# Kernel optimization log

Hardware: AMD Instinct MI355X
Metric: run time of the kernel (lower is better)

The kernel has to match this reference:

```python
import jax, jax.numpy as jnp
import numpy as np

# Dims: M=batch, T=time frames, B=bottleneck channels, H=intermediate channels, KK=kernel size
M, T, B, H, KK = 8, 4000, 128, 512, 3
DILATION = 2
EPS = 1e-8  # gLN eps (ConvTasNet convention)


def prelu(x, a):
    return jnp.where(x >= 0, x, a * x)


def gln(x, gamma, beta):
    # global layer norm over (time, channel) per sample; x: [M, T, C]
    m = jnp.mean(x, axis=(1, 2), keepdims=True)
    v = jnp.mean((x - m) ** 2, axis=(1, 2), keepdims=True)
    return gamma * (x - m) / jnp.sqrt(v + EPS) + beta


def depthwise_conv_same_reflect(x, w):
    # x: [M, C, L], w: [C, K]; dilation 1, 'same' padding with reflect mode
    K = w.shape[1]
    pl = (K - 1) // 2
    xp = jnp.pad(x, ((0, 0), (0, 0), (pl, K - 1 - pl)), mode='reflect')
    return jax.lax.conv_general_dilated(
        xp, w[:, None, :], (1,), 'VALID',
        feature_group_count=x.shape[1], dimension_numbers=('NCH', 'OIH', 'NCH'))


def setup_inputs() -> dict:
    key = jax.random.key(0)
    ks = jax.random.split(key, 12)
    f32 = jnp.float32
    return {
        'x': jax.random.normal(ks[0], (M, T, B), f32),
        'conv1_w': jax.random.normal(ks[1], (H, B), f32) * 0.05,
        'prelu1_a': jnp.asarray(0.25, f32),
        'norm1_g': jnp.ones((H,), f32),
        'norm1_b': jnp.zeros((H,), f32),
        'off_dw_w': jax.random.normal(ks[2], (H, KK), f32) * 0.02,
        'odc_prelu_a': jnp.asarray(0.25, f32),
        'off_pw_w': jax.random.normal(ks[3], (KK, H), f32) * 0.02,
        'opc_prelu_a': jnp.asarray(0.25, f32),
        'dw_w': jax.random.normal(ks[4], (H, KK), f32) * 0.05,
        'dw_b': jax.random.normal(ks[5], (H,), f32) * 0.01,
        'prelu2_a': jnp.asarray(0.25, f32),
        'norm2_g': jnp.ones((H,), f32),
        'norm2_b': jnp.zeros((H,), f32),
        'pw_w': jax.random.normal(ks[6], (B, H), f32) * 0.05,
    }


def reference(x, conv1_w, prelu1_a, norm1_g, norm1_b,
              off_dw_w, odc_prelu_a, off_pw_w, opc_prelu_a,
              dw_w, dw_b, prelu2_a, norm2_g, norm2_b, pw_w):
    dtype = x.dtype
    residual = x
    # 1x1 bottleneck conv -> PReLU -> gLN
    h = jnp.einsum('mtb,hb->mth', x, conv1_w)
    h = gln(prelu(h, prelu1_a), norm1_g, norm1_b)
    hc = jnp.moveaxis(h, 1, 2)  # [M, H, T]

    # --- offset prediction branch (PackedDeformConv1d) ---
    off = depthwise_conv_same_reflect(hc, off_dw_w)          # [M, H, T]
    off = prelu(off, odc_prelu_a)
    off = jnp.einsum('mct,kc->mkt', off, off_pw_w)           # [M, KK, T]
    off = prelu(off, opc_prelu_a)
    offsets = jnp.moveaxis(off, 1, 2)                        # [M, T, KK]

    # --- deformable depthwise conv (same padding, reflect) ---
    pad_tot = DILATION * (KK - 1)
    pl = pad_tot // 2
    xp = jnp.pad(hc, ((0, 0), (0, 0), (pl, pad_tot - pl)), mode='reflect')  # [M,H,Lp]
    Lp = T + pad_tot
    dil_pos = (jnp.arange(KK) * DILATION).astype(dtype)      # [KK]: 0, d, 2d
    t0 = jnp.arange(T, dtype=dtype)[:, None]                 # [T,1]
    Tpos = t0 + dil_pos[None, :] + offsets                   # [M,T,KK]
    Tpos = jnp.clip(Tpos, t0, t0 + dil_pos[-1])              # constrain to receptive field
    U = jnp.clip(jnp.floor(Tpos).astype(jnp.int32), 0, Lp - 2)
    Uf = U.astype(dtype)
    g0 = jax.nn.relu(1.0 - jnp.abs(Uf - Tpos))               # [M,T,KK]
    g1 = jax.nn.relu(1.0 - jnp.abs(Uf + 1.0 - Tpos))
    idx = jnp.broadcast_to(U.reshape(M, 1, T * KK), (M, H, T * KK))
    s0 = jnp.take_along_axis(xp, idx, axis=2).reshape(M, H, T, KK)
    s1 = jnp.take_along_axis(xp, idx + 1, axis=2).reshape(M, H, T, KK)
    sampled = g0[:, None] * s0 + g1[:, None] * s1            # [M,H,T,KK]
    y = jnp.einsum('mhtk,hk->mht', sampled, dw_w) + dw_b[None, :, None]

    # PReLU -> gLN -> 1x1 conv back to B channels, residual add
    y = jnp.moveaxis(y, 1, 2)                                # [M,T,H]
    y = gln(prelu(y, prelu2_a), norm2_g, norm2_b)
    out = jnp.einsum('mth,bh->mtb', y, pw_w)
    return out + residual
```

## Files before the change

### kernel.cpp

```cpp
#include <hip/hip_runtime.h>

#define Mdim 8
#define Tdim 4000
#define Bdim 128
#define Hdim 512
#define NPER (Tdim*Hdim)
#define EPSG 1e-8f
#define ROWS 69

typedef __attribute__((ext_vector_type(8))) short short8;
typedef __attribute__((ext_vector_type(4))) float floatx4;

static __device__ __forceinline__ float bits2f(unsigned short s) {
  union { unsigned int u; float f; } v; v.u = ((unsigned int)s) << 16; return v.f;
}
static __device__ __forceinline__ unsigned short f2bits(float f) {
  union { float f; unsigned int u; } v; v.f = f;
  unsigned int u = v.u;
  u += 0x7fffu + ((u >> 16) & 1u);
  return (unsigned short)(u >> 16);
}
static __device__ __forceinline__ short8 pack8(const float4& a, const float4& b) {
  short8 v;
  v[0]=(short)f2bits(a.x); v[1]=(short)f2bits(a.y); v[2]=(short)f2bits(a.z); v[3]=(short)f2bits(a.w);
  v[4]=(short)f2bits(b.x); v[5]=(short)f2bits(b.y); v[6]=(short)f2bits(b.z); v[7]=(short)f2bits(b.w);
  return v;
}

#define LDS_FENCE() do { \
  asm volatile("s_waitcnt lgkmcnt(0)" ::: "memory"); \
  __builtin_amdgcn_sched_barrier(0); \
} while (0)

__global__ __launch_bounds__(256) void k_prep(
    const float* __restrict__ w1, unsigned short* __restrict__ w1r)
{
  int i = blockIdx.x*256 + threadIdx.x;
  int lane = i & 63, f = i >> 6;
  int nt = f & 3, ks = (f >> 2) & 3, hc = f >> 4;
  int h = hc*64 + nt*16 + (lane & 15);
  int c = ks*32 + (lane >> 4)*8;
  const float* src = &w1[(size_t)h*Bdim + c];
  float4 a = *(const float4*)src;
  float4 b = *(const float4*)(src + 4);
  *(short8*)&w1r[(size_t)i*8] = pack8(a, b);
}

__global__ __launch_bounds__(256) void k_conv1(
    const float* __restrict__ x,
    const unsigned short* __restrict__ w1r,
    const float* __restrict__ a1p,
    unsigned short* __restrict__ Hbuf,
    float2* __restrict__ part1)
{
  __shared__ __align__(16) unsigned short ltile[64*72];
  __shared__ float red[512];

  const int tid = threadIdx.x;
  const int t0 = blockIdx.x * 64;
  const int m  = blockIdx.y;
  const int lane = tid & 63, wv = tid >> 6, quad = lane >> 4, l16 = lane & 15;
  int tr = t0 + wv*16 + l16;
  int trc = tr < Tdim ? tr : Tdim-1;
  const float* xrow = x + ((size_t)m*Tdim + trc)*Bdim;
  short8 afr[4];
  #pragma unroll
  for (int ks = 0; ks < 4; ++ks) {
    float4 fa = *(const float4*)&xrow[ks*32 + quad*8];
    float4 fb = *(const float4*)&xrow[ks*32 + quad*8 + 4];
    afr[ks] = pack8(fa, fb);
  }

  const float a1 = a1p[0];
  const short8* wf = (const short8*)w1r + lane;
  float lsum = 0.f, lss = 0.f;

  for (int hc = 0; hc < 8; ++hc) {
    floatx4 acc[4] = {};
    #pragma unroll
    for (int ks = 0; ks < 4; ++ks)
      #pragma unroll
      for (int nt = 0; nt < 4; ++nt)
        acc[nt] = __builtin_amdgcn_mfma_f32_16x16x32_bf16(
            afr[ks], wf[(hc*16 + ks*4 + nt)*64], acc[nt], 0, 0, 0);

    #pragma unroll
    for (int nt = 0; nt < 4; ++nt) {
      int hl = nt*16 + l16;
      #pragma unroll
      for (int r = 0; r < 4; ++r) {
        int tl = wv*16 + quad*4 + r;
        float v = acc[nt][r];
        v = v >= 0.f ? v : a1 * v;
        if (t0 + tl < Tdim) { lsum += v; lss += v*v; }
        ltile[tl*72 + hl] = f2bits(v);
      }
    }
    LDS_FENCE();
    {
      int tr2 = tid >> 2, ck = (tid & 3) * 16;
      int tg = t0 + tr2;
      if (tg < Tdim) {
        unsigned short* dst = &Hbuf[((size_t)m*Tdim + tg)*Hdim + hc*64 + ck];
        *(short8*)&dst[0] = *(const short8*)&ltile[tr2*72 + ck];
        *(short8*)&dst[8] = *(const short8*)&ltile[tr2*72 + ck + 8];
      }
    }
    LDS_FENCE();
  }

  red[tid] = lsum; red[256 + tid] = lss;
  __syncthreads();
  for (int s = 128; s > 0; s >>= 1) {
    if (tid < s) { red[tid] += red[tid + s]; red[256+tid] += red[256+tid+s]; }
    __syncthreads();
  }
  if (tid == 0)
    part1[(size_t)m*63 + blockIdx.x] = make_float2(red[0], red[256]);
}

__global__ __launch_bounds__(256) void k_deform(
    const unsigned short* __restrict__ Hbuf,
    const float2* __restrict__ part1,
    const float* __restrict__ g1w,
    const float* __restrict__ b1w,
    const float* __restrict__ odw,
    const float* __restrict__ aodcp,
    const float* __restrict__ opw,
    const float* __restrict__ aopcp,
    const float* __restrict__ dww,
    const float* __restrict__ dwb,
    const float* __restrict__ a2p,
    unsigned short* __restrict__ Ybuf,
    float2* __restrict__ part2)
{
  __shared__ __align__(16) unsigned short tile[ROWS*512];
  __shared__ float s_stats[2];
  __shared__ float rsum[4], rss[4];
  const int tid = threadIdx.x, lane = tid & 63, w = tid >> 6;
  const int t0 = blockIdx.x * 64;
  const int m = blockIdx.y;
  const int c8 = lane*8;
  const unsigned short* base = Hbuf + (size_t)m*Tdim*Hdim;

  short8 stg[17];
  #pragma unroll
  for (int i = 0; i < 17; ++i) {
    int s = t0 - 2 + w + i*4;
    s = s < 0 ? -s : s;
    if (s > Tdim-1) s = 2*(Tdim-1) - s;
    stg[i] = *(const short8*)&base[(size_t)s*Hdim + c8];
  }
  short8 extra;
  if (w == 0) {
    int s = t0 + 66;
    if (s > Tdim-1) s = 2*(Tdim-1) - s;
    extra = *(const short8*)&base[(size_t)s*Hdim + c8];
  }

  if (tid < 64) {
    float s = 0.f, q = 0.f;
    if (lane < 63) { float2 p = part1[(size_t)m*63 + lane]; s = p.x; q = p.y; }
    #pragma unroll
    for (int st = 32; st > 0; st >>= 1) { s += __shfl_xor(s, st); q += __shfl_xor(q, st); }
    if (lane == 0) { s_stats[0] = s; s_stats[1] = q; }
  }

  #pragma unroll
  for (int i = 0; i < 17; ++i)
    *(short8*)&tile[(w + i*4)*512 + c8] = stg[i];
  if (w == 0) *(short8*)&tile[68*512 + c8] = extra;

  __syncthreads();

  const float invn = 1.0f/(float)NPER;
  const float mean1 = s_stats[0]*invn;
  const float var1  = fmaxf(s_stats[1]*invn - mean1*mean1, 0.f);
  const float inv1  = 1.0f/sqrtf(var1 + EPSG);

  const float aodc = aodcp[0], aopc = aopcp[0], a2 = a2p[0];
  float wod[24], q0v[8], q1v[8], q2v[8], wd[24], bv[8], Ax[8], Cx[8];
  #pragma unroll
  for (int j = 0; j < 8; j += 4) {
    *(float4*)&q0v[j] = *(const float4*)&opw[c8 + j];
    *(float4*)&q1v[j] = *(const float4*)&opw[Hdim + c8 + j];
    *(float4*)&q2v[j] = *(const float4*)&opw[2*Hdim + c8 + j];
    *(float4*)&bv[j]  = *(const float4*)&dwb[c8 + j];
  }
  #pragma unroll
  for (int j = 0; j < 24; j += 4) {
    *(float4*)&wod[j] = *(const float4*)&odw[c8*3 + j];
    *(float4*)&wd[j]  = *(const float4*)&dww[c8*3 + j];
  }
  #pragma unroll
  for (int j = 0; j < 8; ++j) {
    Ax[j] = g1w[c8 + j] * inv1;
    Cx[j] = b1w[c8 + j] - mean1*Ax[j];
  }

  float lsum = 0.f, lss = 0.f;
  #pragma unroll 1
  for (int it = 0; it < 16; it += 2) {
    const int t = t0 + w*16 + it;
    if (t >= Tdim) break;
    const int sb = t - t0 + 2;

    short8 hrow[2][3];
    #pragma unroll
    for (int tt = 0; tt < 2; ++tt)
      #pragma unroll
      for (int k = 0; k < 3; ++k)
        hrow[tt][k] = *(const short8*)&tile[(sb + tt - 1 + k)*512 + c8];

    float oa[2][3] = {};
    #pragma unroll
    for (int j = 0; j < 8; ++j) {
      float A = Ax[j], C = Cx[j];
      #pragma unroll
      for (int tt = 0; tt < 2; ++tt) {
        float fm = fmaf(A, bits2f((unsigned short)hrow[tt][0][j]), C);
        float fz = fmaf(A, bits2f((unsigned short)hrow[tt][1][j]), C);
        float fp = fmaf(A, bits2f((unsigned short)hrow[tt][2][j]), C);
        float d = fm*wod[j*3+0] + fz*wod[j*3+1] + fp*wod[j*3+2];
        d = d >= 0.f ? d : aodc*d;
        oa[tt][0] = fmaf(d, q0v[j], oa[tt][0]);
        oa[tt][1] = fmaf(d, q1v[j], oa[tt][1]);
        oa[tt][2] = fmaf(d, q2v[j], oa[tt][2]);
      }
    }
    #pragma unroll
    for (int st = 32; st > 0; st >>= 1) {
      #pragma unroll
      for (int tt = 0; tt < 2; ++tt) {
        oa[tt][0] += __shfl_xor(oa[tt][0], st);
        oa[tt][1] += __shfl_xor(oa[tt][1], st);
        oa[tt][2] += __shfl_xor(oa[tt][2], st);
      }
    }

    int S0[2][3], S1[2][3]; float G0[2][3], G1[2][3], GS[2][3];
    #pragma unroll
    for (int tt = 0; tt < 2; ++tt) {
      const float tf = (float)(t + tt);
      #pragma unroll
      for (int k = 0; k < 3; ++k) {
        float off = oa[tt][k];
        off = off >= 0.f ? off : aopc*off;
        float pos = tf + (float)(2*k) + off;
        pos = fminf(fmaxf(pos, tf), tf + 4.0f);
        int U = (int)floorf(pos);
        if (U > Tdim + 2) U = Tdim + 2;
        float Uf = (float)U;
        G0[tt][k] = fmaxf(0.f, 1.f - fabsf(Uf - pos));
        G1[tt][k] = fmaxf(0.f, 1.f - fabsf(Uf + 1.f - pos));
        GS[tt][k] = G0[tt][k] + G1[tt][k];
        S0[tt][k] = U - t0;
        S1[tt][k] = U - t0 + 1;
      }
    }

    short8 s0v[2][3], s1v[2][3];
    #pragma unroll
    for (int tt = 0; tt < 2; ++tt)
      #pragma unroll
      for (int k = 0; k < 3; ++k) {
        s0v[tt][k] = *(const short8*)&tile[S0[tt][k]*512 + c8];
        s1v[tt][k] = *(const short8*)&tile[S1[tt][k]*512 + c8];
      }

    short8 yv[2];
    #pragma unroll
    for (int j = 0; j < 8; ++j) {
      float A = Ax[j], C = Cx[j];
      float w0 = wd[j*3+0], w1 = wd[j*3+1], w2 = wd[j*3+2];
      #pragma unroll
      for (int tt = 0; tt < 2; ++tt) {
        float ybase = fmaf(C, w0*GS[tt][0] + w1*GS[tt][1] + w2*GS[tt][2], bv[j]);
        float t0s = fmaf(G1[tt][0], bits2f((unsigned short)s1v[tt][0][j]), G0[tt][0]*bits2f((unsigned short)s0v[tt][0][j]));
        float t1s = fmaf(G1[tt][1], bits2f((unsigned short)s1v[tt][1][j]), G0[tt][1]*bits2f((unsigned short)s0v[tt][1][j]));
        float t2s = fmaf(G1[tt][2], bits2f((unsigned short)s1v[tt][2][j]), G0[tt][2]*bits2f((unsigned short)s0v[tt][2][j]));
        float acc2 = w0*t0s + w1*t1s + w2*t2s;
        float y = fmaf(A, acc2, ybase);
        float p = y >= 0.f ? y : a2*y;
        lsum += p; lss += p*p;
        yv[tt][j] = (short)f2bits(p);
      }
    }
    #pragma unroll
    for (int tt = 0; tt < 2; ++tt)
      *(short8*)&Ybuf[((size_t)m*Tdim + t + tt)*Hdim + c8] = yv[tt];
  }

  #pragma unroll
  for (int st = 32; st > 0; st >>= 1) {
    lsum += __shfl_xor(lsum, st);
    lss  += __shfl_xor(lss, st);
  }
  if (lane == 0) { rsum[w] = lsum; rss[w] = lss; }
  __syncthreads();
  if (tid == 0)
    part2[(size_t)m*63 + blockIdx.x] =
      make_float2(rsum[0]+rsum[1]+rsum[2]+rsum[3], rss[0]+rss[1]+rss[2]+rss[3]);
}

__global__ __launch_bounds__(64) void k_w2(
    const float2* __restrict__ part2,
    const float* __restrict__ g2w,
    const float* __restrict__ b2w,
    const float* __restrict__ pww,
    unsigned short* __restrict__ W2r,
    float* __restrict__ const2)
{
  const int bid = blockIdx.x;
  const int m = bid >> 7, b = bid & 127;
  const int tid = threadIdx.x;

  float s = 0.f, q = 0.f;
  if (tid < 63) { float2 p = part2[(size_t)m*63 + tid]; s = p.x; q = p.y; }
  #pragma unroll
  for (int st = 32; st > 0; st >>= 1) { s += __shfl_xor(s, st); q += __shfl_xor(q, st); }

  const float invn = 1.0f/(float)NPER;
  const float mean2 = s*invn;
  const float var2  = fmaxf(q*invn - mean2*mean2, 0.f);
  const float inv2  = 1.0f/sqrtf(var2 + EPSG);

  const int j8 = tid*8;
  float g2v[8], b2v[8], pv[8];
  #pragma unroll
  for (int j = 0; j < 8; j += 4) {
    *(float4*)&g2v[j] = *(const float4*)&g2w[j8 + j];
    *(float4*)&b2v[j] = *(const float4*)&b2w[j8 + j];
    *(float4*)&pv[j]  = *(const float4*)&pww[(size_t)b*Hdim + j8 + j];
  }
  float csum = 0.f;
  short8 wv8;
  #pragma unroll
  for (int j = 0; j < 8; ++j) {
    float A = g2v[j] * inv2;
    float C = b2v[j] - mean2*A;
    csum = fmaf(C, pv[j], csum);
    wv8[j] = (short)f2bits(A*pv[j]);
  }
  {
    int half = b >> 6, nt = (b >> 4) & 3, l16 = b & 15;
    int kc = tid >> 4, ks = (tid >> 2) & 3, quad = tid & 3;
    int lane = quad*16 + l16;
    size_t f = ((((size_t)(m*2 + half)*4 + kc)*4 + ks)*4 + nt);
    *(short8*)&W2r[(f*64 + lane)*8] = wv8;
  }

  #pragma unroll
  for (int st = 32; st > 0; st >>= 1) csum += __shfl_down(csum, st);
  if (tid == 0) const2[m*Bdim + b] = csum;
}

__global__ __launch_bounds__(256) void k_out(
    const unsigned short* __restrict__ Ybuf,
    const unsigned short* __restrict__ W2r,
    const float* __restrict__ const2,
    const float* __restrict__ x,
    float* __restrict__ out)
{
  __shared__ __align__(16) float ltf[64*68];
  const int tid = threadIdx.x;
  const int t0 = blockIdx.x*64;
  const int half = blockIdx.y;
  const int n0 = half*64;
  const int m  = blockIdx.z;
  const int lane = tid & 63, wv = tid >> 6, quad = lane >> 4, l16 = lane & 15;
  int tr = t0 + wv*16 + l16;
  int trc = tr < Tdim ? tr : Tdim-1;
  const unsigned short* arow = Ybuf + ((size_t)m*Tdim + trc)*Hdim;
  const short8* wf = (const short8*)W2r + (size_t)(m*2 + half)*64*64 + lane;

  floatx4 acc[4] = {};
  #pragma unroll
  for (int kc = 0; kc < 4; ++kc)
    #pragma unroll
    for (int ks = 0; ks < 4; ++ks) {
      short8 afr = *(const short8*)&arow[kc*128 + ks*32 + quad*8];
      #pragma unroll
      for (int nt = 0; nt < 4; ++nt)
        acc[nt] = __builtin_amdgcn_mfma_f32_16x16x32_bf16(
            afr, wf[((kc*4 + ks)*4 + nt)*64], acc[nt], 0, 0, 0);
    }

  #pragma unroll
  for (int nt = 0; nt < 4; ++nt) {
    int bl = nt*16 + l16;
    float cb = const2[m*Bdim + n0 + bl];
    #pragma unroll
    for (int r = 0; r < 4; ++r) {
      int tl = wv*16 + quad*4 + r;
      ltf[tl*68 + bl] = acc[nt][r] + cb;
    }
  }
  LDS_FENCE();
  {
    int tr2 = tid >> 2, ck = (tid & 3) * 16;
    int tg = t0 + tr2;
    if (tg < Tdim) {
      const float* xr = &x[((size_t)m*Tdim + tg)*Bdim + n0 + ck];
      float* orow = &out[((size_t)m*Tdim + tg)*Bdim + n0 + ck];
      #pragma unroll
      for (int j = 0; j < 4; ++j) {
        float4 v = *(const float4*)&ltf[tr2*68 + ck + j*4];
        float4 rx = *(const float4*)&xr[j*4];
        v.x += rx.x; v.y += rx.y; v.z += rx.z; v.w += rx.w;
        *(float4*)&orow[j*4] = v;
      }
    }
  }
}

extern "C" void kernel_launch(void* const* d_in, const int* in_sizes, int n_in,
                              void* d_out, int out_size, void* d_ws, size_t ws_size,
                              hipStream_t stream)
{
  (void)in_sizes; (void)n_in; (void)out_size; (void)ws_size;
  const float* x    = (const float*)d_in[0];
  const float* w1   = (const float*)d_in[1];
  const float* a1   = (const float*)d_in[2];
  const float* g1   = (const float*)d_in[3];
  const float* b1   = (const float*)d_in[4];
  const float* odw  = (const float*)d_in[5];
  const float* aodc = (const float*)d_in[6];
  const float* opw  = (const float*)d_in[7];
  const float* aopc = (const float*)d_in[8];
  const float* dww  = (const float*)d_in[9];
  const float* dwb  = (const float*)d_in[10];
  const float* a2   = (const float*)d_in[11];
  const float* g2   = (const float*)d_in[12];
  const float* b2   = (const float*)d_in[13];
  const float* pww  = (const float*)d_in[14];
  float* out = (float*)d_out;

  char* ws = (char*)d_ws;
  const size_t OFF_P1  = 0;
  const size_t OFF_C2  = 4096;
  const size_t OFF_P2  = 8192;
  const size_t OFF_W1R = 12288;
  const size_t OFF_W2  = 143360;
  const size_t OFF_H   = 1191936;
  const size_t OFF_Y   = 33959936;
  float2* part1  = (float2*)(ws + OFF_P1);
  float*  const2 = (float*)(ws + OFF_C2);
  float2* part2  = (float2*)(ws + OFF_P2);
  unsigned short* w1r  = (unsigned short*)(ws + OFF_W1R);
  unsigned short* W2r  = (unsigned short*)(ws + OFF_W2);
  unsigned short* Hbuf = (unsigned short*)(ws + OFF_H);
  unsigned short* Ybuf = (unsigned short*)(ws + OFF_Y);

  k_prep  <<<dim3(32), 256, 0, stream>>>(w1, w1r);
  k_conv1 <<<dim3(63, 8), 256, 0, stream>>>(x, w1r, a1, Hbuf, part1);
  k_deform<<<dim3(63, 8), 256, 0, stream>>>(Hbuf, part1, g1, b1, odw, aodc, opw, aopc, dww, dwb, a2, Ybuf, part2);
  k_w2    <<<dim3(1024), 64, 0, stream>>>(part2, g2, b2, pww, W2r, const2);
  k_out   <<<dim3(63, 2, 8), 256, 0, stream>>>(Ybuf, W2r, const2, x, out);
}
```

Baseline: 169.9 us.

## Split deformable stage into offset-MFMA and sampling kernels with more blocks

The monolithic deform kernel is split into a per-sample stats kernel, an offset-prediction kernel that runs the 512-to-3 pointwise projection on MFMA with precomputed folded weights, and a sampling kernel gridded at 500 blocks per sample that reads taps from a buffer and gathers directly from global memory. conv1 is also regridded to 32-row tiles (125 blocks per sample) with per-wave LDS tiles, raising parallelism and dropping the shuffle-heavy reductions. The cost is extra launches, a taps buffer round-trip, and unshared global gathers instead of an LDS tile.

```diff
diff --git a/kernel.cpp b/kernel.cpp
--- a/kernel.cpp
+++ b/kernel.cpp
@@ -6,7 +6,6 @@
 #define Hdim 512
 #define NPER (Tdim*Hdim)
 #define EPSG 1e-8f
-#define ROWS 69
 
 typedef __attribute__((ext_vector_type(8))) short short8;
 typedef __attribute__((ext_vector_type(4))) float floatx4;
@@ -33,17 +32,35 @@
 } while (0)
 
 __global__ __launch_bounds__(256) void k_prep(
-    const float* __restrict__ w1, unsigned short* __restrict__ w1r)
-{
-  int i = blockIdx.x*256 + threadIdx.x;
-  int lane = i & 63, f = i >> 6;
-  int nt = f & 3, ks = (f >> 2) & 3, hc = f >> 4;
-  int h = hc*64 + nt*16 + (lane & 15);
-  int c = ks*32 + (lane >> 4)*8;
-  const float* src = &w1[(size_t)h*Bdim + c];
-  float4 a = *(const float4*)src;
-  float4 b = *(const float4*)(src + 4);
-  *(short8*)&w1r[(size_t)i*8] = pack8(a, b);
+    const float* __restrict__ w1, const float* __restrict__ opw,
+    unsigned short* __restrict__ w1r, unsigned short* __restrict__ opwr)
+{
+  const int tid = threadIdx.x;
+  if (blockIdx.x < 32) {
+    int i = blockIdx.x*256 + tid;
+    int lane = i & 63, f = i >> 6;
+    int nt = f & 3, ks = (f >> 2) & 3, hc = f >> 4;
+    int h = hc*64 + nt*16 + (lane & 15);
+    int c = ks*32 + (lane >> 4)*8;
+    const float* src = &w1[(size_t)h*Bdim + c];
+    float4 a = *(const float4*)src;
+    float4 b = *(const float4*)(src + 4);
+    *(short8*)&w1r[(size_t)i*8] = pack8(a, b);
+  } else {
+    #pragma unroll
+    for (int it = 0; it < 4; ++it) {
+      int idx = it*256 + tid;
+      int ks = idx >> 6, lane = idx & 63;
+      int l16 = lane & 15, q = lane >> 4;
+      int h = ks*32 + q*8;
+      float4 a = make_float4(0.f,0.f,0.f,0.f), b = a;
+      if (l16 < 3) {
+        a = *(const float4*)&opw[(size_t)l16*Hdim + h];
+        b = *(const float4*)&opw[(size_t)l16*Hdim + h + 4];
+      }
+      *(short8*)&opwr[(size_t)idx*8] = pack8(a, b);
+    }
+  }
 }
 
 __global__ __launch_bounds__(256) void k_conv1(
@@ -53,16 +70,16 @@
     unsigned short* __restrict__ Hbuf,
     float2* __restrict__ part1)
 {
-  __shared__ __align__(16) unsigned short ltile[64*72];
+  __shared__ __align__(16) unsigned short ltile[4][16*72];
   __shared__ float red[512];
 
   const int tid = threadIdx.x;
-  const int t0 = blockIdx.x * 64;
+  const int t0 = blockIdx.x * 32;
   const int m  = blockIdx.y;
-  const int lane = tid & 63, wv = tid >> 6, quad = lane >> 4, l16 = lane & 15;
-  int tr = t0 + wv*16 + l16;
-  int trc = tr < Tdim ? tr : Tdim-1;
-  const float* xrow = x + ((size_t)m*Tdim + trc)*Bdim;
+  const int lane = tid & 63, w = tid >> 6, quad = lane >> 4, l16 = lane & 15;
+  const int tsub = w & 1, hh = w >> 1;
+  const int tbase = t0 + tsub*16;
+  const float* xrow = x + ((size_t)m*Tdim + tbase + l16)*Bdim;
   short8 afr[4];
   #pragma unroll
   for (int ks = 0; ks < 4; ++ks) {
@@ -75,36 +92,35 @@
   const short8* wf = (const short8*)w1r + lane;
   float lsum = 0.f, lss = 0.f;
 
-  for (int hc = 0; hc < 8; ++hc) {
+  #pragma unroll
+  for (int hc4 = 0; hc4 < 4; ++hc4) {
+    const int hcg = hh*4 + hc4;
     floatx4 acc[4] = {};
     #pragma unroll
     for (int ks = 0; ks < 4; ++ks)
       #pragma unroll
       for (int nt = 0; nt < 4; ++nt)
         acc[nt] = __builtin_amdgcn_mfma_f32_16x16x32_bf16(
-            afr[ks], wf[(hc*16 + ks*4 + nt)*64], acc[nt], 0, 0, 0);
+            afr[ks], wf[(hcg*16 + ks*4 + nt)*64], acc[nt], 0, 0, 0);
 
     #pragma unroll
     for (int nt = 0; nt < 4; ++nt) {
       int hl = nt*16 + l16;
       #pragma unroll
       for (int r = 0; r < 4; ++r) {
-        int tl = wv*16 + quad*4 + r;
+        int tl = quad*4 + r;
         float v = acc[nt][r];
         v = v >= 0.f ? v : a1 * v;
-        if (t0 + tl < Tdim) { lsum += v; lss += v*v; }
-        ltile[tl*72 + hl] = f2bits(v);
+        lsum += v; lss += v*v;
+        ltile[w][tl*72 + hl] = f2bits(v);
       }
     }
     LDS_FENCE();
     {
-      int tr2 = tid >> 2, ck = (tid & 3) * 16;
-      int tg = t0 + tr2;
-      if (tg < Tdim) {
-        unsigned short* dst = &Hbuf[((size_t)m*Tdim + tg)*Hdim + hc*64 + ck];
-        *(short8*)&dst[0] = *(const short8*)&ltile[tr2*72 + ck];
-        *(short8*)&dst[8] = *(const short8*)&ltile[tr2*72 + ck + 8];
-      }
+      int row = lane >> 2, ck = (lane & 3) * 16;
+      unsigned short* dst = &Hbuf[((size_t)m*Tdim + tbase + row)*Hdim + hcg*64 + ck];
+      *(short8*)&dst[0] = *(const short8*)&ltile[w][row*72 + ck];
+      *(short8*)&dst[8] = *(const short8*)&ltile[w][row*72 + ck + 8];
     }
     LDS_FENCE();
   }
@@ -116,180 +132,188 @@
     __syncthreads();
   }
   if (tid == 0)
-    part1[(size_t)m*63 + blockIdx.x] = make_float2(red[0], red[256]);
-}
-
-__global__ __launch_bounds__(256) void k_deform(
-    const unsigned short* __restrict__ Hbuf,
+    part1[(size_t)m*125 + blockIdx.x] = make_float2(red[0], red[256]);
+}
+
+__global__ __launch_bounds__(128) void k_stats1(
     const float2* __restrict__ part1,
     const float* __restrict__ g1w,
     const float* __restrict__ b1w,
     const float* __restrict__ odw,
+    float2* __restrict__ axcx,
+    float4* __restrict__ wodc)
+{
+  const int m = blockIdx.x, tid = threadIdx.x, lane = tid & 63, w = tid >> 6;
+  __shared__ float sh[4];
+  float s = 0.f, q = 0.f;
+  if (tid < 125) { float2 p = part1[(size_t)m*125 + tid]; s = p.x; q = p.y; }
+  #pragma unroll
+  for (int st = 32; st > 0; st >>= 1) { s += __shfl_xor(s, st); q += __shfl_xor(q, st); }
+  if (lane == 0) { sh[w*2] = s; sh[w*2+1] = q; }
+  __syncthreads();
+  const float S = sh[0] + sh[2], Q = sh[1] + sh[3];
+  const float invn = 1.0f/(float)NPER;
+  const float mean1 = S*invn;
+  const float var1  = fmaxf(Q*invn - mean1*mean1, 0.f);
+  const float inv1  = 1.0f/sqrtf(var1 + EPSG);
+  #pragma unroll
+  for (int i = 0; i < 4; ++i) {
+    int h = tid*4 + i;
+    float A = g1w[h]*inv1;
+    float C = b1w[h] - mean1*A;
+    axcx[(size_t)m*Hdim + h] = make_float2(A, C);
+    float w0 = odw[h*3], w1_ = odw[h*3+1], w2 = odw[h*3+2];
+    wodc[(size_t)m*Hdim + h] = make_float4(A*w0, A*w1_, A*w2, C*(w0+w1_+w2));
+  }
+}
+
+__global__ __launch_bounds__(256) void k_offs(
+    const unsigned short* __restrict__ Hbuf,
+    const float4* __restrict__ wodc,
+    const unsigned short* __restrict__ opwr,
     const float* __restrict__ aodcp,
-    const float* __restrict__ opw,
     const float* __restrict__ aopcp,
+    float4* __restrict__ taps)
+{
+  const int tid = threadIdx.x, lane = tid & 63, w = tid >> 6;
+  const int quad = lane >> 4, l16 = lane & 15;
+  const int m = blockIdx.y;
+  const int tbase = blockIdx.x*64 + w*16;
+  int t = tbase + l16;
+  int tc = t < Tdim ? t : Tdim-1;
+  int tm1 = tc == 0 ? 1 : tc-1;
+  int tp1 = tc == Tdim-1 ? Tdim-2 : tc+1;
+  const unsigned short* r0p = Hbuf + ((size_t)m*Tdim + tm1)*Hdim;
+  const unsigned short* r1p = Hbuf + ((size_t)m*Tdim + tc )*Hdim;
+  const unsigned short* r2p = Hbuf + ((size_t)m*Tdim + tp1)*Hdim;
+  const float4* wcb = wodc + (size_t)m*Hdim;
+  const float aodc = aodcp[0], aopc = aopcp[0];
+
+  floatx4 acc = {};
+  #pragma unroll
+  for (int g = 0; g < 4; ++g) {
+    short8 h0v[4], h1v[4], h2v[4], bop[4];
+    #pragma unroll
+    for (int k2 = 0; k2 < 4; ++k2) {
+      int hc = (g*4 + k2)*32 + quad*8;
+      h0v[k2] = *(const short8*)&r0p[hc];
+      h1v[k2] = *(const short8*)&r1p[hc];
+      h2v[k2] = *(const short8*)&r2p[hc];
+      bop[k2] = *(const short8*)&opwr[(size_t)((g*4 + k2)*64 + lane)*8];
+    }
+    #pragma unroll
+    for (int k2 = 0; k2 < 4; ++k2) {
+      int hc = (g*4 + k2)*32 + quad*8;
+      float d[8];
+      #pragma unroll
+      for (int j = 0; j < 8; ++j) {
+        float4 wc = wcb[hc + j];
+        float dv = fmaf(wc.x, bits2f((unsigned short)h0v[k2][j]),
+                   fmaf(wc.y, bits2f((unsigned short)h1v[k2][j]),
+                   fmaf(wc.z, bits2f((unsigned short)h2v[k2][j]), wc.w)));
+        d[j] = dv >= 0.f ? dv : aodc*dv;
+      }
+      short8 afr = pack8(make_float4(d[0],d[1],d[2],d[3]),
+                         make_float4(d[4],d[5],d[6],d[7]));
+      acc = __builtin_amdgcn_mfma_f32_16x16x32_bf16(afr, bop[k2], acc, 0, 0, 0);
+    }
+  }
+
+  if (l16 < 3) {
+    #pragma unroll
+    for (int r = 0; r < 4; ++r) {
+      int tout = tbase + quad*4 + r;
+      if (tout < Tdim) {
+        float off = acc[r];
+        off = off >= 0.f ? off : aopc*off;
+        float tf = (float)tout;
+        float pos = tf + (float)(2*l16) + off;
+        pos = fminf(fmaxf(pos, tf), tf + 4.0f);
+        int U = (int)floorf(pos);
+        if (U > Tdim + 2) U = Tdim + 2;
+        float Uf = (float)U;
+        float g0 = fmaxf(0.f, 1.f - fabsf(Uf - pos));
+        float g1 = fmaxf(0.f, 1.f - fabsf(Uf + 1.f - pos));
+        int ia = U - 2; ia = ia < 0 ? -ia : ia; if (ia > Tdim-1) ia = 2*(Tdim-1) - ia;
+        int ib = U - 1; ib = ib < 0 ? -ib : ib; if (ib > Tdim-1) ib = 2*(Tdim-1) - ib;
+        taps[((size_t)m*Tdim + tout)*3 + l16] =
+            make_float4(g0, g1, __int_as_float(ia), __int_as_float(ib));
+      }
+    }
+  }
+}
+
+__global__ __launch_bounds__(256) void k_samp(
+    const unsigned short* __restrict__ Hbuf,
+    const float4* __restrict__ taps,
+    const float2* __restrict__ axcx,
     const float* __restrict__ dww,
     const float* __restrict__ dwb,
     const float* __restrict__ a2p,
     unsigned short* __restrict__ Ybuf,
     float2* __restrict__ part2)
 {
-  __shared__ __align__(16) unsigned short tile[ROWS*512];
-  __shared__ float s_stats[2];
   __shared__ float rsum[4], rss[4];
   const int tid = threadIdx.x, lane = tid & 63, w = tid >> 6;
-  const int t0 = blockIdx.x * 64;
+  const int tb = blockIdx.x*8 + w*2;
   const int m = blockIdx.y;
   const int c8 = lane*8;
   const unsigned short* base = Hbuf + (size_t)m*Tdim*Hdim;
 
-  short8 stg[17];
-  #pragma unroll
-  for (int i = 0; i < 17; ++i) {
-    int s = t0 - 2 + w + i*4;
-    s = s < 0 ? -s : s;
-    if (s > Tdim-1) s = 2*(Tdim-1) - s;
-    stg[i] = *(const short8*)&base[(size_t)s*Hdim + c8];
-  }
-  short8 extra;
-  if (w == 0) {
-    int s = t0 + 66;
-    if (s > Tdim-1) s = 2*(Tdim-1) - s;
-    extra = *(const short8*)&base[(size_t)s*Hdim + c8];
-  }
-
-  if (tid < 64) {
-    float s = 0.f, q = 0.f;
-    if (lane < 63) { float2 p = part1[(size_t)m*63 + lane]; s = p.x; q = p.y; }
-    #pragma unroll
-    for (int st = 32; st > 0; st >>= 1) { s += __shfl_xor(s, st); q += __shfl_xor(q, st); }
-    if (lane == 0) { s_stats[0] = s; s_stats[1] = q; }
-  }
-
-  #pragma unroll
-  for (int i = 0; i < 17; ++i)
-    *(short8*)&tile[(w + i*4)*512 + c8] = stg[i];
-  if (w == 0) *(short8*)&tile[68*512 + c8] = extra;
-
-  __syncthreads();
-
-  const float invn = 1.0f/(float)NPER;
-  const float mean1 = s_stats[0]*invn;
-  const float var1  = fmaxf(s_stats[1]*invn - mean1*mean1, 0.f);
-  const float inv1  = 1.0f/sqrtf(var1 + EPSG);
-
-  const float aodc = aodcp[0], aopc = aopcp[0], a2 = a2p[0];
-  float wod[24], q0v[8], q1v[8], q2v[8], wd[24], bv[8], Ax[8], Cx[8];
-  #pragma unroll
-  for (int j = 0; j < 8; j += 4) {
-    *(float4*)&q0v[j] = *(const float4*)&opw[c8 + j];
-    *(float4*)&q1v[j] = *(const float4*)&opw[Hdim + c8 + j];
-    *(float4*)&q2v[j] = *(const float4*)&opw[2*Hdim + c8 + j];
-    *(float4*)&bv[j]  = *(const float4*)&dwb[c8 + j];
-  }
-  #pragma unroll
-  for (int j = 0; j < 24; j += 4) {
-    *(float4*)&wod[j] = *(const float4*)&odw[c8*3 + j];
-    *(float4*)&wd[j]  = *(const float4*)&dww[c8*3 + j];
-  }
+  const float4* tp = taps + ((size_t)m*Tdim + tb)*3;
+  float4 tq[6];
+  #pragma unroll
+  for (int i = 0; i < 6; ++i) tq[i] = tp[i];
+
+  float G0[2][3], G1[2][3], GS[2][3];
+  short8 s0v[2][3], s1v[2][3];
+  #pragma unroll
+  for (int tt = 0; tt < 2; ++tt)
+    #pragma unroll
+    for (int k = 0; k < 3; ++k) {
+      float4 q = tq[tt*3 + k];
+      G0[tt][k] = q.x; G1[tt][k] = q.y; GS[tt][k] = q.x + q.y;
+      int ia = __float_as_int(q.z), ib = __float_as_int(q.w);
+      s0v[tt][k] = *(const short8*)&base[(size_t)ia*Hdim + c8];
+      s1v[tt][k] = *(const short8*)&base[(size_t)ib*Hdim + c8];
+    }
+
+  float wd[24], bv[8], Ax[8], Cx[8];
+  #pragma unroll
+  for (int j = 0; j < 24; j += 4)
+    *(float4*)&wd[j] = *(const float4*)&dww[c8*3 + j];
+  #pragma unroll
+  for (int j = 0; j < 8; j += 4)
+    *(float4*)&bv[j] = *(const float4*)&dwb[c8 + j];
+  #pragma unroll
+  for (int j = 0; j < 8; j += 2) {
+    float4 ac = *(const float4*)&axcx[(size_t)m*Hdim + c8 + j];
+    Ax[j] = ac.x; Cx[j] = ac.y; Ax[j+1] = ac.z; Cx[j+1] = ac.w;
+  }
+  const float a2 = a2p[0];
+
+  float lsum = 0.f, lss = 0.f;
+  short8 yv[2];
   #pragma unroll
   for (int j = 0; j < 8; ++j) {
-    Ax[j] = g1w[c8 + j] * inv1;
-    Cx[j] = b1w[c8 + j] - mean1*Ax[j];
-  }
-
-  float lsum = 0.f, lss = 0.f;
-  #pragma unroll 1
-  for (int it = 0; it < 16; it += 2) {
-    const int t = t0 + w*16 + it;
-    if (t >= Tdim) break;
-    const int sb = t - t0 + 2;
-
-    short8 hrow[2][3];
-    #pragma unroll
-    for (int tt = 0; tt < 2; ++tt)
-      #pragma unroll
-      for (int k = 0; k < 3; ++k)
-        hrow[tt][k] = *(const short8*)&tile[(sb + tt - 1 + k)*512 + c8];
-
-    float oa[2][3] = {};
-    #pragma unroll
-    for (int j = 0; j < 8; ++j) {
-      float A = Ax[j], C = Cx[j];
-      #pragma unroll
-      for (int tt = 0; tt < 2; ++tt) {
-        float fm = fmaf(A, bits2f((unsigned short)hrow[tt][0][j]), C);
-        float fz = fmaf(A, bits2f((unsigned short)hrow[tt][1][j]), C);
-        float fp = fmaf(A, bits2f((unsigned short)hrow[tt][2][j]), C);
-        float d = fm*wod[j*3+0] + fz*wod[j*3+1] + fp*wod[j*3+2];
-        d = d >= 0.f ? d : aodc*d;
-        oa[tt][0] = fmaf(d, q0v[j], oa[tt][0]);
-        oa[tt][1] = fmaf(d, q1v[j], oa[tt][1]);
-        oa[tt][2] = fmaf(d, q2v[j], oa[tt][2]);
-      }
-    }
-    #pragma unroll
-    for (int st = 32; st > 0; st >>= 1) {
-      #pragma unroll
-      for (int tt = 0; tt < 2; ++tt) {
-        oa[tt][0] += __shfl_xor(oa[tt][0], st);
-        oa[tt][1] += __shfl_xor(oa[tt][1], st);
-        oa[tt][2] += __shfl_xor(oa[tt][2], st);
-      }
-    }
-
-    int S0[2][3], S1[2][3]; float G0[2][3], G1[2][3], GS[2][3];
+    float A = Ax[j], C = Cx[j];
+    float w0 = wd[j*3+0], w1 = wd[j*3+1], w2 = wd[j*3+2];
     #pragma unroll
     for (int tt = 0; tt < 2; ++tt) {
-      const float tf = (float)(t + tt);
-      #pragma unroll
-      for (int k = 0; k < 3; ++k) {
-        float off = oa[tt][k];
-        off = off >= 0.f ? off : aopc*off;
-        float pos = tf + (float)(2*k) + off;
-        pos = fminf(fmaxf(pos, tf), tf + 4.0f);
-        int U = (int)floorf(pos);
-        if (U > Tdim + 2) U = Tdim + 2;
-        float Uf = (float)U;
-        G0[tt][k] = fmaxf(0.f, 1.f - fabsf(Uf - pos));
-        G1[tt][k] = fmaxf(0.f, 1.f - fabsf(Uf + 1.f - pos));
-        GS[tt][k] = G0[tt][k] + G1[tt][k];
-        S0[tt][k] = U - t0;
-        S1[tt][k] = U - t0 + 1;
-      }
-    }
-
-    short8 s0v[2][3], s1v[2][3];
-    #pragma unroll
-    for (int tt = 0; tt < 2; ++tt)
-      #pragma unroll
-      for (int k = 0; k < 3; ++k) {
-        s0v[tt][k] = *(const short8*)&tile[S0[tt][k]*512 + c8];
-        s1v[tt][k] = *(const short8*)&tile[S1[tt][k]*512 + c8];
-      }
-
-    short8 yv[2];
-    #pragma unroll
-    for (int j = 0; j < 8; ++j) {
-      float A = Ax[j], C = Cx[j];
-      float w0 = wd[j*3+0], w1 = wd[j*3+1], w2 = wd[j*3+2];
-      #pragma unroll
-      for (int tt = 0; tt < 2; ++tt) {
-        float ybase = fmaf(C, w0*GS[tt][0] + w1*GS[tt][1] + w2*GS[tt][2], bv[j]);
-        float t0s = fmaf(G1[tt][0], bits2f((unsigned short)s1v[tt][0][j]), G0[tt][0]*bits2f((unsigned short)s0v[tt][0][j]));
-        float t1s = fmaf(G1[tt][1], bits2f((unsigned short)s1v[tt][1][j]), G0[tt][1]*bits2f((unsigned short)s0v[tt][1][j]));
-        float t2s = fmaf(G1[tt][2], bits2f((unsigned short)s1v[tt][2][j]), G0[tt][2]*bits2f((unsigned short)s0v[tt][2][j]));
-        float acc2 = w0*t0s + w1*t1s + w2*t2s;
-        float y = fmaf(A, acc2, ybase);
-        float p = y >= 0.f ? y : a2*y;
-        lsum += p; lss += p*p;
-        yv[tt][j] = (short)f2bits(p);
-      }
-    }
-    #pragma unroll
-    for (int tt = 0; tt < 2; ++tt)
-      *(short8*)&Ybuf[((size_t)m*Tdim + t + tt)*Hdim + c8] = yv[tt];
-  }
+      float ybase = fmaf(C, w0*GS[tt][0] + w1*GS[tt][1] + w2*GS[tt][2], bv[j]);
+      float t0s = fmaf(G1[tt][0], bits2f((unsigned short)s1v[tt][0][j]), G0[tt][0]*bits2f((unsigned short)s0v[tt][0][j]));
+      float t1s = fmaf(G1[tt][1], bits2f((unsigned short)s1v[tt][1][j]), G0[tt][1]*bits2f((unsigned short)s0v[tt][1][j]));
+      float t2s = fmaf(G1[tt][2], bits2f((unsigned short)s1v[tt][2][j]), G0[tt][2]*bits2f((unsigned short)s0v[tt][2][j]));
+      float acc2 = w0*t0s + w1*t1s + w2*t2s;
+      float y = fmaf(A, acc2, ybase);
+      float p = y >= 0.f ? y : a2*y;
+      lsum += p; lss += p*p;
+      yv[tt][j] = (short)f2bits(p);
+    }
+  }
+  #pragma unroll
+  for (int tt = 0; tt < 2; ++tt)
+    *(short8*)&Ybuf[((size_t)m*Tdim + tb + tt)*Hdim + c8] = yv[tt];
 
   #pragma unroll
   for (int st = 32; st > 0; st >>= 1) {
@@ -299,7 +323,7 @@
   if (lane == 0) { rsum[w] = lsum; rss[w] = lss; }
   __syncthreads();
   if (tid == 0)
-    part2[(size_t)m*63 + blockIdx.x] =
+    part2[(size_t)m*500 + blockIdx.x] =
       make_float2(rsum[0]+rsum[1]+rsum[2]+rsum[3], rss[0]+rss[1]+rss[2]+rss[3]);
 }
 
@@ -316,7 +340,10 @@
   const int tid = threadIdx.x;
 
   float s = 0.f, q = 0.f;
-  if (tid < 63) { float2 p = part2[(size_t)m*63 + tid]; s = p.x; q = p.y; }
+  for (int i = tid; i < 500; i += 64) {
+    float2 p = part2[(size_t)m*500 + i];
+    s += p.x; q += p.y;
+  }
   #pragma unroll
   for (int st = 32; st > 0; st >>= 1) { s += __shfl_xor(s, st); q += __shfl_xor(q, st); }
 
@@ -437,24 +464,34 @@
   float* out = (float*)d_out;
 
   char* ws = (char*)d_ws;
-  const size_t OFF_P1  = 0;
-  const size_t OFF_C2  = 4096;
-  const size_t OFF_P2  = 8192;
-  const size_t OFF_W1R = 12288;
-  const size_t OFF_W2  = 143360;
-  const size_t OFF_H   = 1191936;
-  const size_t OFF_Y   = 33959936;
+  const size_t OFF_P1   = 0;
+  const size_t OFF_P2   = 8192;
+  const size_t OFF_C2   = 40960;
+  const size_t OFF_AXCX = 45056;
+  const size_t OFF_WODC = 77824;
+  const size_t OFF_W1R  = 143360;
+  const size_t OFF_OPWR = 274432;
+  const size_t OFF_TAPS = 290816;
+  const size_t OFF_W2   = 1826816;
+  const size_t OFF_H    = 2875392;
+  const size_t OFF_Y    = 35643392;
   float2* part1  = (float2*)(ws + OFF_P1);
+  float2* part2  = (float2*)(ws + OFF_P2);
   float*  const2 = (float*)(ws + OFF_C2);
-  float2* part2  = (float2*)(ws + OFF_P2);
+  float2* axcx   = (float2*)(ws + OFF_AXCX);
+  float4* wodc   = (float4*)(ws + OFF_WODC);
   unsigned short* w1r  = (unsigned short*)(ws + OFF_W1R);
+  unsigned short* opwr = (unsigned short*)(ws + OFF_OPWR);
+  float4* taps   = (float4*)(ws + OFF_TAPS);
   unsigned short* W2r  = (unsigned short*)(ws + OFF_W2);
   unsigned short* Hbuf = (unsigned short*)(ws + OFF_H);
   unsigned short* Ybuf = (unsigned short*)(ws + OFF_Y);
 
-  k_prep  <<<dim3(32), 256, 0, stream>>>(w1, w1r);
-  k_conv1 <<<dim3(63, 8), 256, 0, stream>>>(x, w1r, a1, Hbuf, part1);
-  k_deform<<<dim3(63, 8), 256, 0, stream>>>(Hbuf, part1, g1, b1, odw, aodc, opw, aopc, dww, dwb, a2, Ybuf, part2);
+  k_prep  <<<dim3(33), 256, 0, stream>>>(w1, opw, w1r, opwr);
+  k_conv1 <<<dim3(125, 8), 256, 0, stream>>>(x, w1r, a1, Hbuf, part1);
+  k_stats1<<<dim3(8), 128, 0, stream>>>(part1, g1, b1, odw, axcx, wodc);
+  k_offs  <<<dim3(63, 8), 256, 0, stream>>>(Hbuf, wodc, opwr, aodc, aopc, taps);
+  k_samp  <<<dim3(500, 8), 256, 0, stream>>>(Hbuf, taps, axcx, dww, dwb, a2, Ybuf, part2);
   k_w2    <<<dim3(1024), 64, 0, stream>>>(part2, g2, b2, pww, W2r, const2);
   k_out   <<<dim3(63, 2, 8), 256, 0, stream>>>(Ybuf, W2r, const2, x, out);
 }
```

New measurement: 185.1 us. +8.9%, slower.
